# Optimization experiments

Hardware: AMD Instinct MI355X
Metric: run time of the kernel (lower is better)

Reference implementation:

```python
import jax, jax.numpy as jnp
import numpy as np

N_NODES = 50000
E = 800000
NODE_NF = 128
EDGE_NF = 64
IN_NF = NODE_NF + EDGE_NF  # 192
H_NF = 256
OUT_NF = 128


def setup_inputs() -> dict:
    key = jax.random.key(0)
    k1, k2, k3, k4, k5 = jax.random.split(key, 5)
    node_feats = jax.random.normal(k1, (N_NODES, NODE_NF), dtype=jnp.float32)
    edge_index = jax.random.randint(k2, (2, E), 0, N_NODES, dtype=jnp.int64)
    edge_attr = jax.random.normal(k3, (E, EDGE_NF), dtype=jnp.float32)
    # MLP params (Linear stores weight [out, in]; we keep [in, out] for x @ W)
    s1 = 1.0 / np.sqrt(IN_NF)
    s2 = 1.0 / np.sqrt(H_NF)
    W1 = jax.random.uniform(k4, (IN_NF, H_NF), minval=-s1, maxval=s1, dtype=jnp.float32)
    b1 = jnp.zeros((H_NF,), dtype=jnp.float32)
    W2 = jax.random.uniform(k5, (H_NF, OUT_NF), minval=-s2, maxval=s2, dtype=jnp.float32)
    b2 = jnp.zeros((OUT_NF,), dtype=jnp.float32)
    return {"node_feats": node_feats, "edge_index": edge_index, "edge_attr": edge_attr,
            "W1": W1, "b1": b1, "W2": W2, "b2": b2}


def reference(node_feats, edge_index, edge_attr, W1, b1, W2, b2):
    row = edge_index[0]
    # unsorted_segment_sum: scatter-add edge_attr rows into per-node buckets
    agg = jax.ops.segment_sum(edge_attr, row, num_segments=node_feats.shape[0])  # [N, edge_nf]
    node_in = jnp.concatenate([node_feats, agg], axis=1)  # [N, in_nf]
    h = jax.nn.relu(node_in @ W1 + b1)
    return h @ W2 + b2
```

## Files before the change

kernel.cpp:

```cpp
#include <hip/hip_runtime.h>
#include <hip/hip_bf16.h>

typedef unsigned short u16;
typedef unsigned int u32;
typedef __attribute__((ext_vector_type(8))) short short8;
typedef __attribute__((ext_vector_type(4))) float floatx4;

#define N_NODES 50000
#define E_EDGES 800000
#define NODE_NF 128
#define EDGE_NF 64
#define IN_NF 192
#define H_NF 256
#define OUT_NF 128
#define CAP 64

__device__ __forceinline__ float bf2f(u16 u) {
    union { u32 i; float f; } v;
    v.i = ((u32)u) << 16;
    return v.f;
}

__device__ __forceinline__ u16 f2bf(float f) {
    union { float f; u32 i; } v;
    v.f = f;
    u32 b = v.i + 0x7FFF + ((v.i >> 16) & 1);
    return (u16)(b >> 16);
}

__device__ __forceinline__ int probe_bf16_n01(const u32* p, int lane) {
    u32 b = (p[lane] >> 8) & 0x7F;
    return __popcll(__ballot(b == 0x3F)) >= 8;
}
__device__ __forceinline__ int probe_bf16_uni(const u32* p, int lane) {
    u32 b = (p[lane] >> 8) & 0x7F;
    return __popcll(__ballot(b == 60 || b == 61)) >= 8;
}

__global__ void setup_kernel(const void* __restrict__ W1v, const void* __restrict__ W2v,
                             u16* __restrict__ P1, u16* __restrict__ P2,
                             u32* __restrict__ elist) {
    int t = blockIdx.x * 256 + threadIdx.x;
    if (t < 10240) {
        int lane = t & 63;
        int wbf = probe_bf16_uni((const u32*)W1v, lane);
        const u16* W1h = (const u16*)W1v;  const float* W1f = (const float*)W1v;
        const u16* W2h = (const u16*)W2v;  const float* W2f = (const float*)W2v;
        int tile = t >> 6;
        int q = lane >> 4, r = lane & 15;
        u16 v[8];
        if (tile < 96) {
            int kt = tile >> 4, nt = tile & 15;
            int kbase = kt * 32 + q * 8;
            int col = nt * 16 + r;
#pragma unroll
            for (int j = 0; j < 8; ++j) {
                int idx = (kbase + j) * H_NF + col;
                v[j] = wbf ? W1h[idx] : f2bf(W1f[idx]);
            }
            u16* dst = P1 + (size_t)t * 8;
#pragma unroll
            for (int j = 0; j < 8; ++j) dst[j] = v[j];
        } else {
            int t2 = tile - 96;
            int kt = t2 >> 3, ot = t2 & 7;
            int kbase = kt * 32 + q * 8;
            int col = ot * 16 + r;
#pragma unroll
            for (int j = 0; j < 8; ++j) {
                int idx = (kbase + j) * OUT_NF + col;
                v[j] = wbf ? W2h[idx] : f2bf(W2f[idx]);
            }
            u16* dst = P2 + (size_t)(t - 96 * 64) * 8;
#pragma unroll
            for (int j = 0; j < 8; ++j) dst[j] = v[j];
        }
    } else if (t < 10240 + N_NODES) {
        elist[(size_t)(t - 10240) * CAP + (CAP - 1)] = 0;
    }
}

__global__ __launch_bounds__(256) void fill_kernel(const int* __restrict__ eidx,
                                                   u32* __restrict__ elist,
                                                   const void* __restrict__ eav) {
    int t = blockIdx.x * 256 + threadIdx.x;
    int lane = threadIdx.x & 63;
    int eabf = probe_bf16_n01((const u32*)eav, lane);
    u32 hi = (u32)__ballot(lane < 8 && eidx[2 * lane + 1] != 0);
    int is64 = (hi == 0);
    int e = t;
    if (e < E_EDGES) {
        int row = is64 ? (int)(((const long long*)eidx)[e]) : eidx[e];
        row = ((u32)row < (u32)N_NODES) ? row : 0;
        u32* rp = elist + (size_t)row * CAP;
        u32 pos = atomicAdd(rp + (CAP - 1), 1u);
        if (pos < CAP - 1) rp[pos] = e;
    }
    if (t < E_EDGES) {
        const uint4* ep = (const uint4*)eav;
        u32 keep = 0;
#pragma unroll
        for (int i = 0; i < 8; ++i) {
            uint4 v = ep[(size_t)i * E_EDGES + t];
            keep ^= v.x ^ v.w;
        }
        if (!eabf) {
#pragma unroll
            for (int i = 8; i < 16; ++i) {
                uint4 v = ep[(size_t)i * E_EDGES + t];
                keep ^= v.x ^ v.w;
            }
        }
        asm volatile("" :: "v"(keep));
    }
}

__global__ __launch_bounds__(256) void gather_kernel(const void* __restrict__ eav,
                                                     u32* __restrict__ elist) {
    int node = (blockIdx.x * 256 + threadIdx.x) >> 6;
    int lane = threadIdx.x & 63;
    if (node >= N_NODES) return;
    int eabf = probe_bf16_n01((const u32*)eav, lane);
    u32* row = elist + (size_t)node * CAP;
    int deg = (int)row[CAP - 1];
    deg = deg < (CAP - 1) ? deg : (CAP - 1);
    u32 eid = row[lane];
    const u16* eah = (const u16*)eav;
    const float* eaf = (const float*)eav;

    float acc = 0.f;
    if (deg > 0) {
        if (eabf) {
            for (int j = 0; j < deg; j += 8) {
                float v[8];
#pragma unroll
                for (int k = 0; k < 8; ++k) {
                    int idx = j + k;
                    int e = __shfl((int)eid, idx < deg ? idx : deg - 1);
                    v[k] = bf2f(eah[(size_t)e * EDGE_NF + lane]);
                }
#pragma unroll
                for (int k = 0; k < 8; ++k)
                    if (j + k < deg) acc += v[k];
            }
        } else {
            for (int j = 0; j < deg; j += 8) {
                float v[8];
#pragma unroll
                for (int k = 0; k < 8; ++k) {
                    int idx = j + k;
                    int e = __shfl((int)eid, idx < deg ? idx : deg - 1);
                    v[k] = eaf[(size_t)e * EDGE_NF + lane];
                }
#pragma unroll
                for (int k = 0; k < 8; ++k)
                    if (j + k < deg) acc += v[k];
            }
        }
    }
    ((u16*)row)[lane] = f2bf(acc);
}

__global__ __launch_bounds__(256, 3) void mlp_kernel(
    const void* __restrict__ nfv, const void* __restrict__ aggv,
    const u16* __restrict__ P1, const u16* __restrict__ P2,
    const void* __restrict__ b1v, const void* __restrict__ b2v,
    const void* __restrict__ W1v, void* __restrict__ outv) {
    __shared__ u16 sBuf[64 * 264];
    u16* sA = sBuf;
    u16* sH = sBuf;

    int t = threadIdx.x;
    int base = blockIdx.x * 64;
    int lane = t & 63;
    int nfbf = probe_bf16_n01((const u32*)nfv, lane);
    int wbf  = probe_bf16_uni((const u32*)W1v, lane);
    const u16* nfh = (const u16*)nfv;     const float* nff = (const float*)nfv;
    const u16* aggh = (const u16*)aggv;
    const u16* b1h = (const u16*)b1v;     const float* b1f = (const float*)b1v;
    const u16* b2h = (const u16*)b2v;     const float* b2f = (const float*)b2v;

    int r = t >> 2, part = t & 3;
    int node = base + r;
    int nc = node < N_NODES ? node : (N_NODES - 1);
#pragma unroll
    for (int i = 0; i < 6; ++i) {
        int c8 = (part + 4 * i) * 8;
        uint4 v;
        if (c8 < NODE_NF) {
            if (nfbf) {
                v = *(const uint4*)(nfh + (size_t)nc * NODE_NF + c8);
            } else {
                const float4* np = (const float4*)(nff + (size_t)nc * NODE_NF + c8);
                float4 f0 = np[0], f1 = np[1];
                v.x = (u32)f2bf(f0.x) | ((u32)f2bf(f0.y) << 16);
                v.y = (u32)f2bf(f0.z) | ((u32)f2bf(f0.w) << 16);
                v.z = (u32)f2bf(f1.x) | ((u32)f2bf(f1.y) << 16);
                v.w = (u32)f2bf(f1.z) | ((u32)f2bf(f1.w) << 16);
            }
        } else {
            v = *(const uint4*)(aggh + (size_t)nc * 128 + (c8 - NODE_NF));
        }
        *(uint4*)(sA + r * 200 + c8) = v;
    }
    __syncthreads();

    int wv = t >> 6;
    int q = lane >> 4, rr = lane & 15;

    floatx4 acc1[4][4];
#pragma unroll
    for (int rt = 0; rt < 4; ++rt)
#pragma unroll
        for (int ct = 0; ct < 4; ++ct) acc1[rt][ct] = (floatx4)0.f;

#pragma unroll
    for (int kt = 0; kt < 6; ++kt) {
        short8 a[4];
#pragma unroll
        for (int rt = 0; rt < 4; ++rt)
            a[rt] = *(const short8*)(sA + (rt * 16 + rr) * 200 + kt * 32 + q * 8);
#pragma unroll
        for (int ct = 0; ct < 4; ++ct) {
            int nt = wv * 4 + ct;
            short8 b = *(const short8*)(P1 + ((size_t)(kt * 16 + nt) * 64 + lane) * 8);
#pragma unroll
            for (int rt = 0; rt < 4; ++rt)
                acc1[rt][ct] = __builtin_amdgcn_mfma_f32_16x16x32_bf16(a[rt], b, acc1[rt][ct], 0, 0, 0);
        }
    }
    __syncthreads();

#pragma unroll
    for (int ct = 0; ct < 4; ++ct) {
        int col = (wv * 4 + ct) * 16 + rr;
        float bias = wbf ? bf2f(b1h[col]) : b1f[col];
#pragma unroll
        for (int rt = 0; rt < 4; ++rt)
#pragma unroll
            for (int i = 0; i < 4; ++i) {
                float hv = acc1[rt][ct][i] + bias;
                hv = hv > 0.f ? hv : 0.f;
                sH[(rt * 16 + q * 4 + i) * 264 + col] = f2bf(hv);
            }
    }
    __syncthreads();

    floatx4 acc2[4][2];
#pragma unroll
    for (int rt = 0; rt < 4; ++rt)
#pragma unroll
        for (int ct = 0; ct < 2; ++ct) acc2[rt][ct] = (floatx4)0.f;

#pragma unroll
    for (int kt = 0; kt < 8; ++kt) {
        short8 a[4];
#pragma unroll
        for (int rt = 0; rt < 4; ++rt)
            a[rt] = *(const short8*)(sH + (rt * 16 + rr) * 264 + kt * 32 + q * 8);
#pragma unroll
        for (int ct = 0; ct < 2; ++ct) {
            int ot = wv * 2 + ct;
            short8 b = *(const short8*)(P2 + ((size_t)(kt * 8 + ot) * 64 + lane) * 8);
#pragma unroll
            for (int rt = 0; rt < 4; ++rt)
                acc2[rt][ct] = __builtin_amdgcn_mfma_f32_16x16x32_bf16(a[rt], b, acc2[rt][ct], 0, 0, 0);
        }
    }

#pragma unroll
    for (int ct = 0; ct < 2; ++ct) {
        int col = (wv * 2 + ct) * 16 + rr;
        float bias = wbf ? bf2f(b2h[col]) : b2f[col];
#pragma unroll
        for (int rt = 0; rt < 4; ++rt)
#pragma unroll
            for (int i = 0; i < 4; ++i) {
                int node2 = base + rt * 16 + q * 4 + i;
                if (node2 < N_NODES) {
                    float val = acc2[rt][ct][i] + bias;
                    if (nfbf) ((u16*)outv)[(size_t)node2 * OUT_NF + col] = f2bf(val);
                    else      ((float*)outv)[(size_t)node2 * OUT_NF + col] = val;
                }
            }
    }
}

extern "C" void kernel_launch(void* const* d_in, const int* in_sizes, int n_in,
                              void* d_out, int out_size, void* d_ws, size_t ws_size,
                              hipStream_t stream) {
    const void* nf   = d_in[0];
    const int*  eidx = (const int*)d_in[1];
    const void* ea   = d_in[2];
    const void* W1   = d_in[3];
    const void* b1   = d_in[4];
    const void* W2   = d_in[5];
    const void* b2   = d_in[6];

    char* ws = (char*)d_ws;
    u32*   elist = (u32*)(ws + 256);
    u16*   P1    = (u16*)(ws + 12800256);
    u16*   P2    = (u16*)(ws + 12898560);

    setup_kernel<<<236, 256, 0, stream>>>(W1, W2, P1, P2, elist);
    fill_kernel<<<(E_EDGES + 255) / 256, 256, 0, stream>>>(eidx, elist, ea);
    gather_kernel<<<(N_NODES * 64 + 255) / 256, 256, 0, stream>>>(ea, elist);
    mlp_kernel<<<(N_NODES + 63) / 64, 256, 0, stream>>>(nf, elist,
                                                        P1, P2, b1, b2, W1, d_out);
}
```

Before: 403.0 us.

## Fuse setup, edge bucketing and gather into one persistent kernel with grid barrier

Merges the weight-packing, edge-bucketing and per-node gather kernels into a single persistent kernel of 768 blocks. The phases are separated by an atomic grid-wide barrier, and edge degrees move into a separate memset-initialized array. The kernel drops the old pass that streamed the whole edge_attr tensor without using it. The gather loop now uses grid-stride node iteration and prefetches the next node's degree and edge list. This removes launch gaps and redundant traffic, but relies on all 768 blocks being co-resident for the spin barrier and adds a memset launch.

```diff
diff --git a/kernel.cpp b/kernel.cpp
--- a/kernel.cpp
+++ b/kernel.cpp
@@ -14,6 +14,8 @@
 #define H_NF 256
 #define OUT_NF 128
 #define CAP 64
+#define NBLK 768
+#define NWAVES (NBLK * 4)
 
 __device__ __forceinline__ float bf2f(u16 u) {
     union { u32 i; float f; } v;
@@ -37,12 +39,15 @@
     return __popcll(__ballot(b == 60 || b == 61)) >= 8;
 }
 
-__global__ void setup_kernel(const void* __restrict__ W1v, const void* __restrict__ W2v,
-                             u16* __restrict__ P1, u16* __restrict__ P2,
-                             u32* __restrict__ elist) {
+__global__ __launch_bounds__(256, 4) void fused_kernel(
+    const int* __restrict__ eidx, const void* __restrict__ eav,
+    const void* __restrict__ W1v, const void* __restrict__ W2v,
+    u16* __restrict__ P1, u16* __restrict__ P2,
+    u32* __restrict__ bar, u32* __restrict__ deg, u32* __restrict__ elist) {
     int t = blockIdx.x * 256 + threadIdx.x;
+    int lane = threadIdx.x & 63;
+
     if (t < 10240) {
-        int lane = t & 63;
         int wbf = probe_bf16_uni((const u32*)W1v, lane);
         const u16* W1h = (const u16*)W1v;  const float* W1f = (const float*)W1v;
         const u16* W2h = (const u16*)W2v;  const float* W2f = (const float*)W2v;
@@ -54,10 +59,8 @@
             int kbase = kt * 32 + q * 8;
             int col = nt * 16 + r;
 #pragma unroll
-            for (int j = 0; j < 8; ++j) {
-                int idx = (kbase + j) * H_NF + col;
-                v[j] = wbf ? W1h[idx] : f2bf(W1f[idx]);
-            }
+            for (int j = 0; j < 8; ++j) v[j] = wbf ? W1h[(kbase + j) * H_NF + col]
+                                                   : f2bf(W1f[(kbase + j) * H_NF + col]);
             u16* dst = P1 + (size_t)t * 8;
 #pragma unroll
             for (int j = 0; j < 8; ++j) dst[j] = v[j];
@@ -67,98 +70,87 @@
             int kbase = kt * 32 + q * 8;
             int col = ot * 16 + r;
 #pragma unroll
-            for (int j = 0; j < 8; ++j) {
-                int idx = (kbase + j) * OUT_NF + col;
-                v[j] = wbf ? W2h[idx] : f2bf(W2f[idx]);
-            }
+            for (int j = 0; j < 8; ++j) v[j] = wbf ? W2h[(kbase + j) * OUT_NF + col]
+                                                   : f2bf(W2f[(kbase + j) * OUT_NF + col]);
             u16* dst = P2 + (size_t)(t - 96 * 64) * 8;
 #pragma unroll
             for (int j = 0; j < 8; ++j) dst[j] = v[j];
         }
-    } else if (t < 10240 + N_NODES) {
-        elist[(size_t)(t - 10240) * CAP + (CAP - 1)] = 0;
-    }
-}
-
-__global__ __launch_bounds__(256) void fill_kernel(const int* __restrict__ eidx,
-                                                   u32* __restrict__ elist,
-                                                   const void* __restrict__ eav) {
-    int t = blockIdx.x * 256 + threadIdx.x;
-    int lane = threadIdx.x & 63;
-    int eabf = probe_bf16_n01((const u32*)eav, lane);
-    u32 hi = (u32)__ballot(lane < 8 && eidx[2 * lane + 1] != 0);
-    int is64 = (hi == 0);
-    int e = t;
-    if (e < E_EDGES) {
-        int row = is64 ? (int)(((const long long*)eidx)[e]) : eidx[e];
-        row = ((u32)row < (u32)N_NODES) ? row : 0;
-        u32* rp = elist + (size_t)row * CAP;
-        u32 pos = atomicAdd(rp + (CAP - 1), 1u);
-        if (pos < CAP - 1) rp[pos] = e;
-    }
-    if (t < E_EDGES) {
-        const uint4* ep = (const uint4*)eav;
-        u32 keep = 0;
-#pragma unroll
-        for (int i = 0; i < 8; ++i) {
-            uint4 v = ep[(size_t)i * E_EDGES + t];
-            keep ^= v.x ^ v.w;
-        }
-        if (!eabf) {
-#pragma unroll
-            for (int i = 8; i < 16; ++i) {
-                uint4 v = ep[(size_t)i * E_EDGES + t];
-                keep ^= v.x ^ v.w;
-            }
-        }
-        asm volatile("" :: "v"(keep));
-    }
-}
-
-__global__ __launch_bounds__(256) void gather_kernel(const void* __restrict__ eav,
-                                                     u32* __restrict__ elist) {
-    int node = (blockIdx.x * 256 + threadIdx.x) >> 6;
-    int lane = threadIdx.x & 63;
-    if (node >= N_NODES) return;
-    int eabf = probe_bf16_n01((const u32*)eav, lane);
-    u32* row = elist + (size_t)node * CAP;
-    int deg = (int)row[CAP - 1];
-    deg = deg < (CAP - 1) ? deg : (CAP - 1);
-    u32 eid = row[lane];
-    const u16* eah = (const u16*)eav;
-    const float* eaf = (const float*)eav;
-
-    float acc = 0.f;
-    if (deg > 0) {
-        if (eabf) {
-            for (int j = 0; j < deg; j += 8) {
-                float v[8];
-#pragma unroll
-                for (int k = 0; k < 8; ++k) {
-                    int idx = j + k;
-                    int e = __shfl((int)eid, idx < deg ? idx : deg - 1);
-                    v[k] = bf2f(eah[(size_t)e * EDGE_NF + lane]);
+    }
+
+    {
+        u32 hi = (u32)__ballot(lane < 8 && eidx[2 * lane + 1] != 0);
+        int is64 = (hi == 0);
+        for (int e = t; e < E_EDGES; e += NBLK * 256) {
+            int row = is64 ? (int)(((const long long*)eidx)[e]) : eidx[e];
+            row = ((u32)row < (u32)N_NODES) ? row : 0;
+            u32 pos = atomicAdd(&deg[row], 1u);
+            if (pos < CAP) elist[(size_t)row * CAP + pos] = e;
+        }
+    }
+
+    __syncthreads();
+    if (threadIdx.x == 0) {
+        __threadfence();
+        __hip_atomic_fetch_add(bar, 1u, __ATOMIC_ACQ_REL, __HIP_MEMORY_SCOPE_AGENT);
+        while (__hip_atomic_load(bar, __ATOMIC_ACQUIRE, __HIP_MEMORY_SCOPE_AGENT) < (u32)NBLK)
+            __builtin_amdgcn_s_sleep(2);
+    }
+    __syncthreads();
+
+    {
+        int eabf = probe_bf16_n01((const u32*)eav, lane);
+        const u16* eah = (const u16*)eav;
+        const float* eaf = (const float*)eav;
+        int gw = t >> 6;
+        int node = gw;
+        int dcur = 0; u32 ecur = 0;
+        if (node < N_NODES) {
+            dcur = (int)deg[node];
+            ecur = elist[(size_t)node * CAP + lane];
+        }
+        while (node < N_NODES) {
+            int nn = node + NWAVES;
+            int dn = 0; u32 en = 0;
+            if (nn < N_NODES) {
+                dn = (int)deg[nn];
+                en = elist[(size_t)nn * CAP + lane];
+            }
+            int d = dcur < CAP ? dcur : CAP;
+            float acc = 0.f;
+            if (d > 0) {
+                if (eabf) {
+                    for (int j = 0; j < d; j += 8) {
+                        float v[8];
+#pragma unroll
+                        for (int k = 0; k < 8; ++k) {
+                            int idx = j + k;
+                            int e = __shfl((int)ecur, idx < d ? idx : d - 1);
+                            v[k] = bf2f(eah[(size_t)e * EDGE_NF + lane]);
+                        }
+#pragma unroll
+                        for (int k = 0; k < 8; ++k)
+                            if (j + k < d) acc += v[k];
+                    }
+                } else {
+                    for (int j = 0; j < d; j += 8) {
+                        float v[8];
+#pragma unroll
+                        for (int k = 0; k < 8; ++k) {
+                            int idx = j + k;
+                            int e = __shfl((int)ecur, idx < d ? idx : d - 1);
+                            v[k] = eaf[(size_t)e * EDGE_NF + lane];
+                        }
+#pragma unroll
+                        for (int k = 0; k < 8; ++k)
+                            if (j + k < d) acc += v[k];
+                    }
                 }
-#pragma unroll
-                for (int k = 0; k < 8; ++k)
-                    if (j + k < deg) acc += v[k];
-            }
-        } else {
-            for (int j = 0; j < deg; j += 8) {
-                float v[8];
-#pragma unroll
-                for (int k = 0; k < 8; ++k) {
-                    int idx = j + k;
-                    int e = __shfl((int)eid, idx < deg ? idx : deg - 1);
-                    v[k] = eaf[(size_t)e * EDGE_NF + lane];
-                }
-#pragma unroll
-                for (int k = 0; k < 8; ++k)
-                    if (j + k < deg) acc += v[k];
-            }
-        }
-    }
-    ((u16*)row)[lane] = f2bf(acc);
+            }
+            ((u16*)(elist + (size_t)node * CAP))[lane] = f2bf(acc);
+            node = nn; dcur = dn; ecur = en;
+        }
+    }
 }
 
 __global__ __launch_bounds__(256, 3) void mlp_kernel(
@@ -298,13 +290,14 @@
     const void* b2   = d_in[6];
 
     char* ws = (char*)d_ws;
-    u32*   elist = (u32*)(ws + 256);
-    u16*   P1    = (u16*)(ws + 12800256);
-    u16*   P2    = (u16*)(ws + 12898560);
-
-    setup_kernel<<<236, 256, 0, stream>>>(W1, W2, P1, P2, elist);
-    fill_kernel<<<(E_EDGES + 255) / 256, 256, 0, stream>>>(eidx, elist, ea);
-    gather_kernel<<<(N_NODES * 64 + 255) / 256, 256, 0, stream>>>(ea, elist);
+    u32*   bar   = (u32*)ws;
+    u32*   deg   = (u32*)(ws + 256);
+    u32*   elist = (u32*)(ws + 200704);
+    u16*   P1    = (u16*)(ws + 13000704);
+    u16*   P2    = (u16*)(ws + 13099008);
+
+    hipMemsetAsync(ws, 0, 200704, stream);
+    fused_kernel<<<NBLK, 256, 0, stream>>>(eidx, ea, W1, W2, P1, P2, bar, deg, elist);
     mlp_kernel<<<(N_NODES + 63) / 64, 256, 0, stream>>>(nf, elist,
                                                         P1, P2, b1, b2, W1, d_out);
 }
```

Result: slower. 513.9 us (+27.5%).
